# Optimization experiments

Measured on AMD Instinct MI355X. Metric: run time of the kernel, lower is better.

## Reference

```python
import jax, jax.numpy as jnp
import numpy as np

B = 65536
N_SPARSE = 20
N_VARLEN = 3
SEQ_LEN = 50
VOCAB = 100000
N_DENSE = 13


def setup_inputs() -> dict:
    key = jax.random.key(0)
    k1, k2, k3, k4, k5, k6 = jax.random.split(key, 6)
    sparse_ids = jax.random.randint(k1, (B, N_SPARSE), 0, VOCAB, dtype=jnp.int64 if jax.config.jax_enable_x64 else jnp.int32)
    varlen_ids = jax.random.randint(k2, (B, N_VARLEN, SEQ_LEN), 0, VOCAB, dtype=sparse_ids.dtype)
    dense_x = jax.random.normal(k3, (B, N_DENSE), dtype=jnp.float32)
    # dim-1 embedding table per feature, stacked: [n_feat, vocab]
    sparse_tables = jax.random.normal(k4, (N_SPARSE, VOCAB), dtype=jnp.float32)
    varlen_tables = jax.random.normal(k5, (N_VARLEN, VOCAB), dtype=jnp.float32)
    dense_w = jax.random.normal(k6, (N_DENSE,), dtype=jnp.float32) * 1e-4
    return {
        "sparse_ids": sparse_ids,
        "varlen_ids": varlen_ids,
        "dense_x": dense_x,
        "sparse_tables": sparse_tables,
        "varlen_tables": varlen_tables,
        "dense_w": dense_w,
    }


def reference(sparse_ids, varlen_ids, dense_x, sparse_tables, varlen_tables, dense_w):
    # per-feature dim-1 embedding gather for single-value sparse feats: [B, Fs]
    fs = jnp.arange(N_SPARSE)
    sparse_vals = sparse_tables[fs[None, :], sparse_ids]
    # varlen gather: [B, Fv, L]; mask_zero=True -> id 0 contributes nothing; sum pooling
    fv = jnp.arange(N_VARLEN)
    varlen_vals = varlen_tables[fv[None, :, None], varlen_ids]
    mask = (varlen_ids != 0).astype(varlen_vals.dtype)
    varlen_pool = jnp.sum(varlen_vals * mask, axis=-1)  # [B, Fv]
    # reduce_sum over concat([sparse_vals, varlen_pool]) == sum of both sums
    logit = jnp.sum(sparse_vals, axis=-1) + jnp.sum(varlen_pool, axis=-1)
    # linear dense logit: concat(dense) @ W[:,1], squeezed
    logit = logit + dense_x @ dense_w
    return logit  # [B]
```

## Files before the change

### kernel.cpp

```cpp
#include <hip/hip_runtime.h>

constexpr int B        = 65536;
constexpr int N_SPARSE = 20;
constexpr int N_VARLEN = 3;
constexpr int SEQ_LEN  = 50;
constexpr int VOCAB    = 100000;
constexpr int N_DENSE  = 13;
constexpr int VAR_TOT  = N_VARLEN * SEQ_LEN;

constexpr int NB_VAR    = (B / 2) * 16 / 256;
constexpr int NB_SPARSE = B / 256;

__global__ __launch_bounds__(256) void dense_kernel(
    const float* __restrict__ dense_x,
    const float* __restrict__ dense_w,
    float*       __restrict__ out)
{
    const int row = blockIdx.x * blockDim.x + threadIdx.x;
    if (row >= B) return;
    const float* drow = dense_x + (long)row * N_DENSE;
    float acc = 0.f;
    #pragma unroll
    for (int d = 0; d < N_DENSE; ++d) acc += drow[d] * dense_w[d];
    out[row] = acc;
}

__global__ __launch_bounds__(256) void gather_kernel(
    const int*   __restrict__ sparse_ids,
    const int*   __restrict__ varlen_ids,
    const float* __restrict__ sparse_tables,
    const float* __restrict__ varlen_tables,
    float*       __restrict__ out)
{
    if (blockIdx.x < NB_VAR) {
        const int tid = blockIdx.x * blockDim.x + threadIdx.x;
        const int g   = tid >> 4;
        const int t   = tid & 15;

        const int4* vptr = (const int4*)(varlen_ids) + (long)g * 75;

        int4 vid[5];
        #pragma unroll
        for (int k = 0; k < 4; ++k) vid[k] = vptr[t + 16 * k];
        const bool v5 = (t + 64) < 75;
        if (v5) vid[4] = vptr[t + 64];

        float acc0 = 0.f, acc1 = 0.f;

        #pragma unroll
        for (int k = 0; k < 5; ++k) {
            if (k == 4 && !v5) continue;
            const int s0 = 4 * (t + 16 * k);
            const int ids[4] = { vid[k].x, vid[k].y, vid[k].z, vid[k].w };
            #pragma unroll
            for (int j = 0; j < 4; ++j) {
                const int s  = s0 + j;
                const bool r1 = (s >= VAR_TOT);
                const int p  = r1 ? (s - VAR_TOT) : s;
                const int v  = (p >= 100) ? 2 : (p >= 50 ? 1 : 0);
                const float val = varlen_tables[v * VOCAB + ids[j]];
                const float m   = (ids[j] != 0) ? val : 0.f;
                acc0 += r1 ? 0.f : m;
                acc1 += r1 ? m   : 0.f;
            }
        }

        #pragma unroll
        for (int o = 1; o < 16; o <<= 1) {
            acc0 += __shfl_xor(acc0, o);
            acc1 += __shfl_xor(acc1, o);
        }
        if (t == 0) {
            atomicAdd(out + 2 * g,     acc0);
            atomicAdd(out + 2 * g + 1, acc1);
        }
    } else {
        const int row = (blockIdx.x - NB_VAR) * blockDim.x + threadIdx.x;
        if (row >= B) return;

        const int4* sptr = (const int4*)(sparse_ids) + (long)row * 5;
        int4 sid[5];
        #pragma unroll
        for (int k = 0; k < 5; ++k) sid[k] = sptr[k];

        float acc = 0.f;
        #pragma unroll
        for (int k = 0; k < 5; ++k) {
            const int ids[4] = { sid[k].x, sid[k].y, sid[k].z, sid[k].w };
            #pragma unroll
            for (int j = 0; j < 4; ++j) {
                const int f = 4 * k + j;
                acc += sparse_tables[f * VOCAB + ids[j]];
            }
        }
        atomicAdd(out + row, acc);
    }
}

extern "C" void kernel_launch(void* const* d_in, const int* in_sizes, int n_in,
                              void* d_out, int out_size, void* d_ws, size_t ws_size,
                              hipStream_t stream) {
    const int*   sparse_ids    = (const int*)d_in[0];
    const int*   varlen_ids    = (const int*)d_in[1];
    const float* dense_x       = (const float*)d_in[2];
    const float* sparse_tables = (const float*)d_in[3];
    const float* varlen_tables = (const float*)d_in[4];
    const float* dense_w       = (const float*)d_in[5];
    float*       out           = (float*)d_out;

    dense_kernel<<<B / 256, 256, 0, stream>>>(dense_x, dense_w, out);
    gather_kernel<<<NB_VAR + NB_SPARSE, 256, 0, stream>>>(
        sparse_ids, varlen_ids, sparse_tables, varlen_tables, out);
}
```

Baseline: 137.5 us.

## Fuse dense, sparse and varlen paths into one kernel with per-pair groups

```diff
diff --git a/kernel.cpp b/kernel.cpp
--- a/kernel.cpp
+++ b/kernel.cpp
@@ -8,92 +8,99 @@
 constexpr int N_DENSE  = 13;
 constexpr int VAR_TOT  = N_VARLEN * SEQ_LEN;
 
-constexpr int NB_VAR    = (B / 2) * 16 / 256;
-constexpr int NB_SPARSE = B / 256;
+constexpr int NPAIR = B / 2;
+constexpr int NBLK  = NPAIR * 16 / 256;
 
-__global__ __launch_bounds__(256) void dense_kernel(
+typedef int   v4i __attribute__((ext_vector_type(4)));
+typedef float v2f __attribute__((ext_vector_type(2)));
+
+__global__ __launch_bounds__(256, 4) void fused_kernel(
+    const int*   __restrict__ sparse_ids,
+    const int*   __restrict__ varlen_ids,
     const float* __restrict__ dense_x,
+    const float* __restrict__ sparse_tables,
+    const float* __restrict__ varlen_tables,
     const float* __restrict__ dense_w,
     float*       __restrict__ out)
 {
-    const int row = blockIdx.x * blockDim.x + threadIdx.x;
-    if (row >= B) return;
-    const float* drow = dense_x + (long)row * N_DENSE;
-    float acc = 0.f;
+    const int tid = blockIdx.x * blockDim.x + threadIdx.x;
+    const int g   = tid >> 4;
+    const int t   = tid & 15;
+
+    const v4i* vptr = (const v4i*)(varlen_ids) + (long)g * 75;
+    v4i vid[5];
     #pragma unroll
-    for (int d = 0; d < N_DENSE; ++d) acc += drow[d] * dense_w[d];
-    out[row] = acc;
-}
+    for (int k = 0; k < 4; ++k)
+        vid[k] = __builtin_nontemporal_load(vptr + t + 16 * k);
+    v4i zero4 = {0, 0, 0, 0};
+    vid[4] = zero4;
+    if (t < 11)
+        vid[4] = __builtin_nontemporal_load(vptr + t + 64);
 
-__global__ __launch_bounds__(256) void gather_kernel(
-    const int*   __restrict__ sparse_ids,
-    const int*   __restrict__ varlen_ids,
-    const float* __restrict__ sparse_tables,
-    const float* __restrict__ varlen_tables,
-    float*       __restrict__ out)
-{
-    if (blockIdx.x < NB_VAR) {
-        const int tid = blockIdx.x * blockDim.x + threadIdx.x;
-        const int g   = tid >> 4;
-        const int t   = tid & 15;
+    v4i sid = zero4;
+    const bool sp = (t < 10);
+    if (sp)
+        sid = __builtin_nontemporal_load(
+                  (const v4i*)(sparse_ids) + (long)(2 * g + (t >= 5)) * 5 + (t % 5));
 
-        const int4* vptr = (const int4*)(varlen_ids) + (long)g * 75;
+    const float* dx = dense_x + (long)(2 * g) * N_DENSE;
+    float d0 = 0.f, d1 = 0.f, wt = 0.f;
+    if (t < 13) {
+        d0 = __builtin_nontemporal_load(dx + t);
+        d1 = __builtin_nontemporal_load(dx + 13 + t);
+        wt = dense_w[t];
+    }
 
-        int4 vid[5];
+    float sv0 = 0.f, sv1 = 0.f, sv2 = 0.f, sv3 = 0.f;
+    if (sp) {
+        const int f0 = 4 * (t % 5);
+        sv0 = sparse_tables[(long)(f0 + 0) * VOCAB + sid[0]];
+        sv1 = sparse_tables[(long)(f0 + 1) * VOCAB + sid[1]];
+        sv2 = sparse_tables[(long)(f0 + 2) * VOCAB + sid[2]];
+        sv3 = sparse_tables[(long)(f0 + 3) * VOCAB + sid[3]];
+    }
+
+    float vv[20];
+    #pragma unroll
+    for (int k = 0; k < 5; ++k) {
+        const int c = (k < 4) ? (t + 16 * k) : (t + 64);
         #pragma unroll
-        for (int k = 0; k < 4; ++k) vid[k] = vptr[t + 16 * k];
-        const bool v5 = (t + 64) < 75;
-        if (v5) vid[4] = vptr[t + 64];
+        for (int j = 0; j < 4; ++j) {
+            const int s = 4 * c + j;
+            const int p = (s >= VAR_TOT) ? (s - VAR_TOT) : s;
+            const int v = (p >= 2 * SEQ_LEN) ? 2 : ((p >= SEQ_LEN) ? 1 : 0);
+            vv[4 * k + j] = varlen_tables[(long)v * VOCAB + vid[k][j]];
+        }
+    }
 
-        float acc0 = 0.f, acc1 = 0.f;
+    float acc0 = d0 * wt;
+    float acc1 = d1 * wt;
+    #pragma unroll
+    for (int k = 0; k < 5; ++k) {
+        const int c = (k < 4) ? (t + 16 * k) : (t + 64);
+        #pragma unroll
+        for (int j = 0; j < 4; ++j) {
+            const int  s  = 4 * c + j;
+            const bool r1 = (s >= VAR_TOT);
+            const float m = (vid[k][j] != 0) ? vv[4 * k + j] : 0.f;
+            acc0 += r1 ? 0.f : m;
+            acc1 += r1 ? m   : 0.f;
+        }
+    }
+    const float ssum = sv0 + sv1 + sv2 + sv3;
+    acc0 += (t < 5)  ? ssum : 0.f;
+    acc1 += (t >= 5) ? ssum : 0.f;
 
-        #pragma unroll
-        for (int k = 0; k < 5; ++k) {
-            if (k == 4 && !v5) continue;
-            const int s0 = 4 * (t + 16 * k);
-            const int ids[4] = { vid[k].x, vid[k].y, vid[k].z, vid[k].w };
-            #pragma unroll
-            for (int j = 0; j < 4; ++j) {
-                const int s  = s0 + j;
-                const bool r1 = (s >= VAR_TOT);
-                const int p  = r1 ? (s - VAR_TOT) : s;
-                const int v  = (p >= 100) ? 2 : (p >= 50 ? 1 : 0);
-                const float val = varlen_tables[v * VOCAB + ids[j]];
-                const float m   = (ids[j] != 0) ? val : 0.f;
-                acc0 += r1 ? 0.f : m;
-                acc1 += r1 ? m   : 0.f;
-            }
-        }
-
-        #pragma unroll
-        for (int o = 1; o < 16; o <<= 1) {
-            acc0 += __shfl_xor(acc0, o);
-            acc1 += __shfl_xor(acc1, o);
-        }
-        if (t == 0) {
-            atomicAdd(out + 2 * g,     acc0);
-            atomicAdd(out + 2 * g + 1, acc1);
-        }
-    } else {
-        const int row = (blockIdx.x - NB_VAR) * blockDim.x + threadIdx.x;
-        if (row >= B) return;
-
-        const int4* sptr = (const int4*)(sparse_ids) + (long)row * 5;
-        int4 sid[5];
-        #pragma unroll
-        for (int k = 0; k < 5; ++k) sid[k] = sptr[k];
-
-        float acc = 0.f;
-        #pragma unroll
-        for (int k = 0; k < 5; ++k) {
-            const int ids[4] = { sid[k].x, sid[k].y, sid[k].z, sid[k].w };
-            #pragma unroll
-            for (int j = 0; j < 4; ++j) {
-                const int f = 4 * k + j;
-                acc += sparse_tables[f * VOCAB + ids[j]];
-            }
-        }
-        atomicAdd(out + row, acc);
+    #pragma unroll
+    for (int o = 1; o < 16; o <<= 1) {
+        acc0 += __shfl_xor(acc0, o);
+        acc1 += __shfl_xor(acc1, o);
+    }
+    if (t == 0) {
+        v2f r;
+        r[0] = acc0;
+        r[1] = acc1;
+        __builtin_nontemporal_store(r, (v2f*)(out + 2 * g));
     }
 }
 
@@ -108,7 +115,6 @@
     const float* dense_w       = (const float*)d_in[5];
     float*       out           = (float*)d_out;
 
-    dense_kernel<<<B / 256, 256, 0, stream>>>(dense_x, dense_w, out);
-    gather_kernel<<<NB_VAR + NB_SPARSE, 256, 0, stream>>>(
-        sparse_ids, varlen_ids, sparse_tables, varlen_tables, out);
+    fused_kernel<<<NBLK, 256, 0, stream>>>(
+        sparse_ids, varlen_ids, dense_x, sparse_tables, varlen_tables, dense_w, out);
 }
```

New measurement: 142.2 us. +3.5%, slower.
